# Kernel optimization log

Hardware: AMD Instinct MI355X
Metric: run time of the kernel (lower is better)

## Reference

```python
import jax, jax.numpy as jnp
import numpy as np
import math

NUM_HEADS = 8
LN_EPS = 1e-5


def layer_norm(x, g, b):
    mu = x.mean(-1, keepdims=True)
    var = ((x - mu) ** 2).mean(-1, keepdims=True)
    return (x - mu) * jax.lax.rsqrt(var + LN_EPS) * g + b


def typed_linear(x, W, types):
    # x: [E, in], W: [R, in, out], types: [E] int -> [E, out]
    out = jnp.zeros((x.shape[0], W.shape[-1]), x.dtype)
    for r in range(W.shape[0]):  # small fixed relation count
        out = out + jnp.where((types == r)[:, None], x @ W[r], 0.0)
    return out


def setup_inputs() -> dict:
    key = jax.random.key(0)
    ks = jax.random.split(key, 20)
    N, M, E = 50000, 10000, 100000
    in_dim, e_dim, out_dim, td = 128, 32, 128, 32
    R, T = 8, 4
    inp = {
        'src_h': jax.random.normal(ks[0], (N, in_dim), jnp.float32),
        'src_tw': jax.random.normal(ks[1], (N, td), jnp.float32),
        'src_tb': jax.random.normal(ks[2], (N, td), jnp.float32),
        'edge_h': jax.random.normal(ks[3], (E, e_dim), jnp.float32),
        'date': jax.random.uniform(ks[4], (E,), jnp.float32),
        'src_idx': jax.random.randint(ks[5], (E,), 0, N, jnp.int32),
        'dst_idx': jax.random.randint(ks[6], (E,), 0, M, jnp.int32),
        'etype': jax.random.randint(ks[7], (E,), 0, R, jnp.int32),
        'ntype': jax.random.randint(ks[8], (M,), 0, T, jnp.int32),
    }
    def w(k, shape):
        return jax.random.normal(k, shape, jnp.float32) / math.sqrt(shape[-2])
    inp['Wq'] = w(ks[9], (R, in_dim, out_dim))
    inp['Wk'] = w(ks[10], (R, in_dim + e_dim, out_dim))
    inp['Wv'] = w(ks[11], (R, in_dim + e_dim, out_dim))
    inp['Wa'] = w(ks[12], (T, out_dim, out_dim))
    inp['h_bias'] = jnp.zeros((T, out_dim), jnp.float32)
    inp['skip'] = jnp.ones((T,), jnp.float32)
    inp['src_ln_g'] = jnp.ones((in_dim + e_dim,), jnp.float32)
    inp['src_ln_b'] = jnp.zeros((in_dim + e_dim,), jnp.float32)
    inp['dst_ln_g'] = jnp.ones((in_dim,), jnp.float32)
    inp['dst_ln_b'] = jnp.zeros((in_dim,), jnp.float32)
    return inp


def reference(src_h, src_tw, src_tb, edge_h, date, src_idx, dst_idx, etype, ntype,
              Wq, Wk, Wv, Wa, h_bias, skip, src_ln_g, src_ln_b, dst_ln_g, dst_ln_b):
    M = ntype.shape[0]
    out_dim = Wq.shape[-1]
    H = NUM_HEADS
    hs = out_dim // H
    td = src_tw.shape[-1]
    t = date[:, None]  # [E,1]

    # gather src / dst node data per edge (dst nodes are first M src rows)
    h_s, tw_s, tb_s = src_h[src_idx], src_tw[src_idx], src_tb[src_idx]
    h_d, tw_d, tb_d = src_h[dst_idx], src_tw[dst_idx], src_tb[dst_idx]

    # time2vec modulation of the first td channels
    dia_s = jnp.concatenate([jnp.sin(tw_s * t + tb_s) * h_s[:, :td], h_s[:, td:]], -1)
    dia_d = jnp.concatenate([jnp.sin(tw_d * t + tb_d) * h_d[:, :td], h_d[:, td:]], -1)
    dia_s = jnp.concatenate([dia_s, edge_h], -1)  # [E, in_dim+e_dim]

    # pre_norm
    dia_s = layer_norm(dia_s, src_ln_g, src_ln_b)
    dia_d = layer_norm(dia_d, dst_ln_g, dst_ln_b)

    q = typed_linear(dia_d, Wq, etype).reshape(-1, H, hs)
    k = typed_linear(dia_s, Wk, etype).reshape(-1, H, hs)
    v = typed_linear(dia_s, Wv, etype).reshape(-1, H, hs)

    a = (q * k).sum(-1) / math.sqrt(out_dim)  # [E, H]

    # edge_softmax: segment softmax over destination nodes
    amax = jax.lax.stop_gradient(jax.ops.segment_max(a, dst_idx, num_segments=M))
    ex = jnp.exp(a - amax[dst_idx])
    denom = jax.ops.segment_sum(ex, dst_idx, num_segments=M)
    alpha = ex / denom[dst_idx]  # [E, H]

    # weighted scatter-sum aggregation
    m = (v * alpha[..., None]).reshape(-1, out_dim)  # [E, out_dim]
    h = jax.ops.segment_sum(m, dst_idx, num_segments=M)  # [M, out_dim]

    h = h + h_bias[ntype]
    gate = jax.nn.sigmoid(skip[ntype])[:, None]
    h = typed_linear(h, Wa, ntype)  # dropout is identity at eval
    dst_h = src_h[:M]
    return h * gate + dst_h * (1.0 - gate)
```

## Files before the change

### kernel.cpp

```cpp
#include <hip/hip_runtime.h>


typedef __attribute__((ext_vector_type(8))) short short8;
typedef __attribute__((ext_vector_type(4))) float f32x4;

__device__ __forceinline__ unsigned short f2bf(float f){
  union { float f; unsigned u; } x; x.f = f;
  unsigned r = x.u + 0x7FFFu + ((x.u >> 16) & 1u);
  return (unsigned short)(r >> 16);
}
__device__ __forceinline__ float bf2f(unsigned short b){
  union { unsigned u; float f; } x; x.u = ((unsigned)b) << 16;
  return x.f;
}
__device__ __forceinline__ float wred(float v){
  #pragma unroll
  for(int i=1;i<64;i<<=1) v += __shfl_xor(v, i);
  return v;
}


__global__ void k_zero(int* __restrict__ p, int n){
  int i = blockIdx.x*256 + threadIdx.x;
  if(i < n) p[i] = 0;
}

__global__ __launch_bounds__(256) void k_hist(
    const int* __restrict__ etype, const int* __restrict__ dst_idx,
    const int* __restrict__ ntype,
    int* cnt_e, int* cnt_d, int* cnt_n, int E, int M){
  __shared__ int le[8], ln[4];
  int tid = threadIdx.x;
  if(tid < 8) le[tid] = 0;
  if(tid < 4) ln[tid] = 0;
  __syncthreads();
  int g = blockIdx.x*256 + tid;
  if(g < E){ atomicAdd(&le[etype[g]], 1); atomicAdd(&cnt_d[dst_idx[g]], 1); }
  if(g < M){ atomicAdd(&ln[ntype[g]], 1); }
  __syncthreads();
  if(tid < 8 && le[tid]) atomicAdd(&cnt_e[tid], le[tid]);
  if(tid < 4 && ln[tid]) atomicAdd(&cnt_n[tid], ln[tid]);
}

__global__ __launch_bounds__(1024) void k_scan(const int* __restrict__ cnt_e, int* off_e,
                                               const int* __restrict__ cnt_n, int* off_n,
                                               const int* __restrict__ cnt_d, int* off_d, int M){
  __shared__ int part[1024];
  int tid = threadIdx.x;
  if(tid == 0){
    int s = 0;
    for(int i=0;i<8;i++){ off_e[i]=s; s+=cnt_e[i]; } off_e[8]=s;
    s = 0;
    for(int i=0;i<4;i++){ off_n[i]=s; s+=cnt_n[i]; } off_n[4]=s;
  }
  int per = (M + 1023) >> 10;
  int s = 0;
  for(int j=0;j<per;j++){ int idx = tid*per + j; if(idx < M) s += cnt_d[idx]; }
  part[tid] = s; __syncthreads();
  for(int o=1;o<1024;o<<=1){
    int v = (tid >= o) ? part[tid-o] : 0;
    __syncthreads();
    part[tid] += v;
    __syncthreads();
  }
  int run = (tid == 0) ? 0 : part[tid-1];
  for(int j=0;j<per;j++){
    int idx = tid*per + j;
    if(idx < M){ off_d[idx] = run; run += cnt_d[idx]; }
  }
  if(tid == 1023) off_d[M] = run;
}

__global__ __launch_bounds__(256) void k_scatter(
    const int* __restrict__ etype, const int* __restrict__ dst_idx,
    const int* __restrict__ ntype,
    const int* __restrict__ off_e, int* cur_e,
    const int* __restrict__ off_d, int* cur_d,
    const int* __restrict__ off_n, int* cur_n,
    int* eperm, int* dstlist, int* nperm, int* npos, int E, int M){
  __shared__ int lcnt[8], lbase[8], lnc[4], lnb[4];
  int tid = threadIdx.x;
  if(tid < 8) lcnt[tid] = 0;
  if(tid < 4) lnc[tid] = 0;
  __syncthreads();
  int g = blockIdx.x*256 + tid;
  int r = 0, lrank = 0, t = 0, nrank = 0;
  bool inE = (g < E), inM = (g < M);
  if(inE){ r = etype[g]; lrank = atomicAdd(&lcnt[r], 1); }
  if(inM){ t = ntype[g]; nrank = atomicAdd(&lnc[t], 1); }
  __syncthreads();
  if(tid < 8 && lcnt[tid]) lbase[tid] = atomicAdd(&cur_e[tid], lcnt[tid]);
  if(tid < 4 && lnc[tid])  lnb[tid]   = atomicAdd(&cur_n[tid], lnc[tid]);
  __syncthreads();
  if(inE){
    int p = off_e[r] + lbase[r] + lrank;
    eperm[p] = g;
    int d = dst_idx[g];
    int q = off_d[d] + atomicAdd(&cur_d[d], 1);
    dstlist[q] = p;
  }
  if(inM){
    int np = off_n[t] + lnb[t] + nrank;
    npos[g] = np;
    nperm[np] = g;
  }
}

__global__ void k_convw(const float* __restrict__ Wq, const float* __restrict__ Wk,
                        const float* __restrict__ Wv, const float* __restrict__ Wa,
                        unsigned short* Wq_t, unsigned short* Wk_t,
                        unsigned short* Wv_t, unsigned short* Wa_t){
  int tid = blockIdx.x*256 + threadIdx.x;
  if(tid < 131072){
    int r = tid >> 14, rem = tid & 16383, i = rem >> 7, o = rem & 127;
    Wq_t[(r<<14) + (o<<7) + i] = f2bf(Wq[tid]);
  } else if(tid < 294912){
    int u = tid - 131072;
    int r = u / 20480, rem = u - r*20480, i = rem >> 7, o = rem & 127;
    Wk_t[r*20480 + o*160 + i] = f2bf(Wk[u]);
  } else if(tid < 458752){
    int u = tid - 294912;
    int r = u / 20480, rem = u - r*20480, i = rem >> 7, o = rem & 127;
    Wv_t[r*20480 + o*160 + i] = f2bf(Wv[u]);
  } else if(tid < 524288){
    int u = tid - 458752;
    int r = u >> 14, rem = u & 16383, i = rem >> 7, o = rem & 127;
    Wa_t[(r<<14) + (o<<7) + i] = f2bf(Wa[u]);
  }
}

__global__ __launch_bounds__(256) void k_prep(
  const float* __restrict__ src_h, const float* __restrict__ src_tw, const float* __restrict__ src_tb,
  const float* __restrict__ edge_h, const float* __restrict__ date,
  const int* __restrict__ src_idx, const int* __restrict__ dst_idx, const int* __restrict__ eperm,
  const float* __restrict__ g_s, const float* __restrict__ b_s,
  const float* __restrict__ g_d, const float* __restrict__ b_d,
  unsigned short* __restrict__ dia_s, unsigned short* __restrict__ dia_d, int E)
{
  int p = blockIdx.x*4 + (threadIdx.x >> 6);
  if(p >= E) return;
  int lane = threadIdx.x & 63;
  int e = eperm[p];
  float t = date[e];
  int s = src_idx[e], d = dst_idx[e];
  {
    float h0 = src_h[(size_t)s*128 + lane];
    float h1 = src_h[(size_t)s*128 + 64 + lane];
    float x0 = h0, x2 = 0.f;
    if(lane < 32){
      x0 = __sinf(src_tw[s*32 + lane]*t + src_tb[s*32 + lane]) * h0;
      x2 = edge_h[(size_t)e*32 + lane];
    }
    float x1 = h1;
    float mu = wred(x0 + x1 + x2) * (1.f/160.f);
    float d0 = x0-mu, d1 = x1-mu, d2 = (lane<32) ? (x2-mu) : 0.f;
    float var = wred(d0*d0 + d1*d1 + d2*d2) * (1.f/160.f);
    float sc = rsqrtf(var + 1e-5f);
    size_t bo = (size_t)p*160;
    dia_s[bo + lane]      = f2bf(d0*sc*g_s[lane]      + b_s[lane]);
    dia_s[bo + 64 + lane] = f2bf(d1*sc*g_s[64+lane]   + b_s[64+lane]);
    if(lane < 32)
      dia_s[bo + 128 + lane] = f2bf(d2*sc*g_s[128+lane] + b_s[128+lane]);
  }
  {
    float h0 = src_h[(size_t)d*128 + lane];
    float h1 = src_h[(size_t)d*128 + 64 + lane];
    float x0 = (lane < 32) ? __sinf(src_tw[d*32+lane]*t + src_tb[d*32+lane]) * h0 : h0;
    float x1 = h1;
    float mu = wred(x0 + x1) * (1.f/128.f);
    float d0 = x0-mu, d1 = x1-mu;
    float var = wred(d0*d0 + d1*d1) * (1.f/128.f);
    float sc = rsqrtf(var + 1e-5f);
    size_t bo = (size_t)p*128;
    dia_d[bo + lane]      = f2bf(d0*sc*g_d[lane]    + b_d[lane]);
    dia_d[bo + 64 + lane] = f2bf(d1*sc*g_d[64+lane] + b_d[64+lane]);
  }
}

__device__ __forceinline__ void gemm64(
  const unsigned short* __restrict__ A, int lda,
  const unsigned short* __restrict__ Wg, int Kd,
  unsigned short* __restrict__ Bt, f32x4* acc, int tid)
{
  int lane = tid & 63, w = tid >> 6, m = lane & 15, quad = lane >> 4;
  #pragma unroll
  for(int i=0;i<8;i++) acc[i] = (f32x4){0.f,0.f,0.f,0.f};
  for(int k0=0; k0<Kd; k0+=32){
    __syncthreads();
    #pragma unroll
    for(int j=0;j<2;j++){
      int idx = j*256 + tid;
      int n = idx >> 2, qc = idx & 3;
      *(int4*)(Bt + n*40 + qc*8) = *(const int4*)(Wg + (size_t)n*Kd + k0 + qc*8);
    }
    __syncthreads();
    short8 b0 = *(const short8*)(Bt + (w*32 +      m)*40 + quad*8);
    short8 b1 = *(const short8*)(Bt + (w*32 + 16 + m)*40 + quad*8);
    #pragma unroll
    for(int rt=0; rt<4; rt++){
      short8 af = *(const short8*)(A + (rt*16 + m)*lda + k0 + quad*8);
      acc[rt*2+0] = __builtin_amdgcn_mfma_f32_16x16x32_bf16(af, b0, acc[rt*2+0], 0,0,0);
      acc[rt*2+1] = __builtin_amdgcn_mfma_f32_16x16x32_bf16(af, b1, acc[rt*2+1], 0,0,0);
    }
  }
}

__global__ __launch_bounds__(256) void k_qkv(
  const unsigned short* __restrict__ dia_d, const unsigned short* __restrict__ dia_s,
  const unsigned short* __restrict__ Wq_t, const unsigned short* __restrict__ Wk_t,
  const unsigned short* __restrict__ Wv_t,
  const int* __restrict__ cnt_e, const int* __restrict__ off_e,
  float* __restrict__ abuf, unsigned short* __restrict__ vbuf)
{
  __shared__ unsigned short Ad[64*136];
  __shared__ unsigned short As[64*168];
  __shared__ unsigned short Bt[128*40];
  int bid = blockIdx.x;
  int r = -1, tl0 = 0, accT = 0;
  #pragma unroll
  for(int i=0;i<8;i++){
    int n = cnt_e[i], tt = (n + 63) >> 6;
    if(r < 0 && bid < accT + tt){ r = i; tl0 = bid - accT; }
    accT += tt;
  }
  if(r < 0) return;
  int row0 = off_e[r] + tl0*64;
  int nv = min(64, cnt_e[r] - tl0*64);
  int tid = threadIdx.x;
  {
    int4 z = make_int4(0,0,0,0);
    #pragma unroll
    for(int it=0; it<4; it++){
      int idx = it*256 + tid, row = idx >> 4, c = idx & 15;
      int4 v = z;
      if(row < nv) v = *(const int4*)(dia_d + (size_t)(row0+row)*128 + c*8);
      *(int4*)(Ad + row*136 + c*8) = v;
    }
    #pragma unroll
    for(int it=0; it<5; it++){
      int idx = it*256 + tid, row = idx/20, c = idx%20;
      int4 v = z;
      if(row < nv) v = *(const int4*)(dia_s + (size_t)(row0+row)*160 + c*8);
      *(int4*)(As + row*168 + c*8) = v;
    }
  }
  int lane = tid & 63, w = tid >> 6, m = lane & 15, quad = lane >> 4;
  f32x4 q[8], kk[8], vv[8];
  gemm64(Ad, 136, Wq_t + r*16384, 128, Bt, q,  tid);
  gemm64(As, 168, Wk_t + r*20480, 160, Bt, kk, tid);
  const float inv = 0.08838834764831845f;
  #pragma unroll
  for(int rt=0; rt<4; rt++)
  #pragma unroll
  for(int ct=0; ct<2; ct++){
    #pragma unroll
    for(int reg=0; reg<4; reg++){
      float s = q[rt*2+ct][reg] * kk[rt*2+ct][reg];
      s += __shfl_xor(s,1); s += __shfl_xor(s,2); s += __shfl_xor(s,4); s += __shfl_xor(s,8);
      int row = rt*16 + quad*4 + reg;
      if(m == 0 && row < nv) abuf[(size_t)(row0+row)*8 + w*2 + ct] = s * inv;
    }
  }
  gemm64(As, 168, Wv_t + r*20480, 160, Bt, vv, tid);
  #pragma unroll
  for(int rt=0; rt<4; rt++)
  #pragma unroll
  for(int ct=0; ct<2; ct++)
  #pragma unroll
  for(int reg=0; reg<4; reg++){
    int row = rt*16 + quad*4 + reg;
    if(row < nv)
      vbuf[(size_t)(row0+row)*128 + w*32 + ct*16 + m] = f2bf(vv[rt*2+ct][reg]);
  }
}

__global__ __launch_bounds__(128) void k_aggr(
  const float* __restrict__ abuf, const unsigned short* __restrict__ vbuf,
  const int* __restrict__ dstlist, const int* __restrict__ off_d,
  const int* __restrict__ npos, const int* __restrict__ ntype,
  const float* __restrict__ h_bias, unsigned short* __restrict__ hpre)
{
  int d = blockIdx.x, tid = threadIdx.x;
  int o0 = off_d[d], cnt = off_d[d+1] - o0;
  __shared__ float den[8];
  if(tid < 8) den[tid] = 0.f;
  __syncthreads();
  for(int idx = tid; idx < cnt*8; idx += 128){
    int i = idx >> 3, h = idx & 7;
    float ex = __expf(abuf[(size_t)dstlist[o0+i]*8 + h]);
    atomicAdd(&den[h], ex);
  }
  __syncthreads();
  int h = tid >> 4;
  float dh = den[h];
  float rd = (dh > 0.f) ? (1.f/dh) : 0.f;
  float acc = 0.f;
  for(int i=0; i<cnt; i++){
    int p = dstlist[o0+i];
    float al = __expf(abuf[(size_t)p*8 + h]) * rd;
    acc += al * bf2f(vbuf[(size_t)p*128 + tid]);
  }
  int t = ntype[d];
  acc += h_bias[t*128 + tid];
  hpre[(size_t)npos[d]*128 + tid] = f2bf(acc);
}

__global__ __launch_bounds__(256) void k_final(
  const unsigned short* __restrict__ hpre, const unsigned short* __restrict__ Wa_t,
  const int* __restrict__ cnt_n, const int* __restrict__ off_n, const int* __restrict__ nperm,
  const float* __restrict__ skip, const float* __restrict__ src_h, float* __restrict__ out)
{
  __shared__ unsigned short Ah[64*136];
  __shared__ unsigned short Bt[128*40];
  int bid = blockIdx.x;
  int r = -1, tl0 = 0, accT = 0;
  #pragma unroll
  for(int i=0;i<4;i++){
    int n = cnt_n[i], tt = (n + 63) >> 6;
    if(r < 0 && bid < accT + tt){ r = i; tl0 = bid - accT; }
    accT += tt;
  }
  if(r < 0) return;
  int row0 = off_n[r] + tl0*64;
  int nv = min(64, cnt_n[r] - tl0*64);
  float gate = 1.f / (1.f + __expf(-skip[r]));
  int tid = threadIdx.x;
  int4 z = make_int4(0,0,0,0);
  #pragma unroll
  for(int it=0; it<4; it++){
    int idx = it*256 + tid, row = idx >> 4, c = idx & 15;
    int4 v = z;
    if(row < nv) v = *(const int4*)(hpre + (size_t)(row0+row)*128 + c*8);
    *(int4*)(Ah + row*136 + c*8) = v;
  }
  f32x4 acc[8];
  gemm64(Ah, 136, Wa_t + r*16384, 128, Bt, acc, tid);
  int lane = tid & 63, w = tid >> 6, m = lane & 15, quad = lane >> 4;
  #pragma unroll
  for(int rt=0; rt<4; rt++)
  #pragma unroll
  for(int ct=0; ct<2; ct++)
  #pragma unroll
  for(int reg=0; reg<4; reg++){
    int row = rt*16 + quad*4 + reg;
    if(row < nv){
      int dd = nperm[row0+row];
      int col = w*32 + ct*16 + m;
      out[(size_t)dd*128 + col] = acc[rt*2+ct][reg]*gate + src_h[(size_t)dd*128 + col]*(1.f - gate);
    }
  }
}

extern "C" void kernel_launch(void* const* d_in, const int* in_sizes, int n_in,
                              void* d_out, int out_size, void* d_ws, size_t ws_size,
                              hipStream_t stream)
{
  const float* src_h  = (const float*)d_in[0];
  const float* src_tw = (const float*)d_in[1];
  const float* src_tb = (const float*)d_in[2];
  const float* edge_h = (const float*)d_in[3];
  const float* date   = (const float*)d_in[4];
  const int*   src_idx= (const int*)d_in[5];
  const int*   dst_idx= (const int*)d_in[6];
  const int*   etype  = (const int*)d_in[7];
  const int*   ntype  = (const int*)d_in[8];
  const float* Wq     = (const float*)d_in[9];
  const float* Wk     = (const float*)d_in[10];
  const float* Wv     = (const float*)d_in[11];
  const float* Wa     = (const float*)d_in[12];
  const float* h_bias = (const float*)d_in[13];
  const float* skip   = (const float*)d_in[14];
  const float* g_s    = (const float*)d_in[15];
  const float* b_s    = (const float*)d_in[16];
  const float* g_d    = (const float*)d_in[17];
  const float* b_d    = (const float*)d_in[18];
  float* out = (float*)d_out;

  const int E = in_sizes[4];
  const int M = in_sizes[8];

  char* base = (char*)d_ws;
  size_t off = 0;
  auto alloc = [&](size_t bytes)->char*{
    off = (off + 255) & ~(size_t)255;
    char* p = base + off; off += bytes; return p;
  };
  int* cnt_e = (int*)alloc((size_t)(24 + 2*M)*4);
  int* cur_e = cnt_e + 8;
  int* cnt_n = cur_e + 8;
  int* cur_n = cnt_n + 4;
  int* cnt_d = cur_n + 4;
  int* cur_d = cnt_d + M;
  const int nzero = 24 + 2*M;
  int* off_e = (int*)alloc(9*4);
  int* off_n = (int*)alloc(5*4);
  int* off_d = (int*)alloc((size_t)(M+1)*4);
  int* eperm   = (int*)alloc((size_t)E*4);
  int* dstlist = (int*)alloc((size_t)E*4);
  int* nperm   = (int*)alloc((size_t)M*4);
  int* npos    = (int*)alloc((size_t)M*4);
  unsigned short* Wq_t = (unsigned short*)alloc((size_t)8*128*128*2);
  unsigned short* Wk_t = (unsigned short*)alloc((size_t)8*160*128*2);
  unsigned short* Wv_t = (unsigned short*)alloc((size_t)8*160*128*2);
  unsigned short* Wa_t = (unsigned short*)alloc((size_t)4*128*128*2);
  unsigned short* dia_d = (unsigned short*)alloc((size_t)E*128*2);
  unsigned short* dia_s = (unsigned short*)alloc((size_t)E*160*2);
  unsigned short* vbuf  = (unsigned short*)alloc((size_t)E*128*2);
  unsigned short* hpre  = (unsigned short*)alloc((size_t)M*128*2);
  float* abuf = (float*)alloc((size_t)E*8*4);

  k_zero<<<dim3((nzero+255)/256), dim3(256), 0, stream>>>(cnt_e, nzero);
  k_hist<<<dim3((E+255)/256), dim3(256), 0, stream>>>(etype, dst_idx, ntype, cnt_e, cnt_d, cnt_n, E, M);
  k_scan<<<dim3(1), dim3(1024), 0, stream>>>(cnt_e, off_e, cnt_n, off_n, cnt_d, off_d, M);
  k_scatter<<<dim3((E+255)/256), dim3(256), 0, stream>>>(etype, dst_idx, ntype,
      off_e, cur_e, off_d, cur_d, off_n, cur_n, eperm, dstlist, nperm, npos, E, M);
  k_convw<<<dim3(2048), dim3(256), 0, stream>>>(Wq, Wk, Wv, Wa, Wq_t, Wk_t, Wv_t, Wa_t);
  k_prep<<<dim3((E+3)/4), dim3(256), 0, stream>>>(src_h, src_tw, src_tb, edge_h, date,
      src_idx, dst_idx, eperm, g_s, b_s, g_d, b_d, dia_s, dia_d, E);
  k_qkv<<<dim3(E/64 + 9), dim3(256), 0, stream>>>(dia_d, dia_s, Wq_t, Wk_t, Wv_t,
      cnt_e, off_e, abuf, vbuf);
  k_aggr<<<dim3(M), dim3(128), 0, stream>>>(abuf, vbuf, dstlist, off_d, npos, ntype, h_bias, hpre);
  k_final<<<dim3(M/64 + 5), dim3(256), 0, stream>>>(hpre, Wa_t, cnt_n, off_n, nperm, skip, src_h, out);
}
```

Measured before the change: 289.8 us.

## Pre-swizzle weights into MFMA fragment layout and load B directly to registers

The weight conversion kernel now writes bf16 weights in the exact per-lane MFMA B-fragment order. The GEMM helper can then load all B fragments straight from global memory into registers with coalesced 16-byte loads, with no LDS staging. This drops the shared-memory B tile and the two barriers per K-step. It adds register pressure, since up to 10 short8 fragments are held per GEMM, and relies on weights being L2-resident across blocks.

```diff
diff --git a/kernel.cpp b/kernel.cpp
--- a/kernel.cpp
+++ b/kernel.cpp
@@ -112,20 +112,24 @@
                         unsigned short* Wv_t, unsigned short* Wa_t){
   int tid = blockIdx.x*256 + threadIdx.x;
   if(tid < 131072){
-    int r = tid >> 14, rem = tid & 16383, i = rem >> 7, o = rem & 127;
-    Wq_t[(r<<14) + (o<<7) + i] = f2bf(Wq[tid]);
+    int r = tid >> 14, rem = tid & 16383, k = rem >> 7, n = rem & 127;
+    int nb=n>>4, m=n&15, c=k>>5, quad=(k>>3)&3, j=k&7;
+    Wq_t[r*16384 + ((nb*4 + c)*4 + quad)*128 + m*8 + j] = f2bf(Wq[tid]);
   } else if(tid < 294912){
     int u = tid - 131072;
-    int r = u / 20480, rem = u - r*20480, i = rem >> 7, o = rem & 127;
-    Wk_t[r*20480 + o*160 + i] = f2bf(Wk[u]);
+    int r = u / 20480, rem = u - r*20480, k = rem >> 7, n = rem & 127;
+    int nb=n>>4, m=n&15, c=k>>5, quad=(k>>3)&3, j=k&7;
+    Wk_t[r*20480 + ((nb*5 + c)*4 + quad)*128 + m*8 + j] = f2bf(Wk[u]);
   } else if(tid < 458752){
     int u = tid - 294912;
-    int r = u / 20480, rem = u - r*20480, i = rem >> 7, o = rem & 127;
-    Wv_t[r*20480 + o*160 + i] = f2bf(Wv[u]);
+    int r = u / 20480, rem = u - r*20480, k = rem >> 7, n = rem & 127;
+    int nb=n>>4, m=n&15, c=k>>5, quad=(k>>3)&3, j=k&7;
+    Wv_t[r*20480 + ((nb*5 + c)*4 + quad)*128 + m*8 + j] = f2bf(Wv[u]);
   } else if(tid < 524288){
     int u = tid - 458752;
-    int r = u >> 14, rem = u & 16383, i = rem >> 7, o = rem & 127;
-    Wa_t[(r<<14) + (o<<7) + i] = f2bf(Wa[u]);
+    int r = u >> 14, rem = u & 16383, k = rem >> 7, n = rem & 127;
+    int nb=n>>4, m=n&15, c=k>>5, quad=(k>>3)&3, j=k&7;
+    Wa_t[r*16384 + ((nb*4 + c)*4 + quad)*128 + m*8 + j] = f2bf(Wa[u]);
   }
 }
 
@@ -177,30 +181,29 @@
   }
 }
 
-__device__ __forceinline__ void gemm64(
+template<int NC>
+__device__ __forceinline__ void gemm64r(
   const unsigned short* __restrict__ A, int lda,
-  const unsigned short* __restrict__ Wg, int Kd,
-  unsigned short* __restrict__ Bt, f32x4* acc, int tid)
+  const unsigned short* __restrict__ Wf,
+  f32x4* acc, int tid)
 {
   int lane = tid & 63, w = tid >> 6, m = lane & 15, quad = lane >> 4;
+  const unsigned short* p0 = Wf + (size_t)(2*w)*NC*512 + lane*8;
+  short8 b0[NC], b1[NC];
+  #pragma unroll
+  for(int c=0;c<NC;c++){
+    b0[c] = *(const short8*)(p0 + c*512);
+    b1[c] = *(const short8*)(p0 + NC*512 + c*512);
+  }
   #pragma unroll
   for(int i=0;i<8;i++) acc[i] = (f32x4){0.f,0.f,0.f,0.f};
-  for(int k0=0; k0<Kd; k0+=32){
-    __syncthreads();
-    #pragma unroll
-    for(int j=0;j<2;j++){
-      int idx = j*256 + tid;
-      int n = idx >> 2, qc = idx & 3;
-      *(int4*)(Bt + n*40 + qc*8) = *(const int4*)(Wg + (size_t)n*Kd + k0 + qc*8);
-    }
-    __syncthreads();
-    short8 b0 = *(const short8*)(Bt + (w*32 +      m)*40 + quad*8);
-    short8 b1 = *(const short8*)(Bt + (w*32 + 16 + m)*40 + quad*8);
+  #pragma unroll
+  for(int c=0;c<NC;c++){
     #pragma unroll
     for(int rt=0; rt<4; rt++){
-      short8 af = *(const short8*)(A + (rt*16 + m)*lda + k0 + quad*8);
-      acc[rt*2+0] = __builtin_amdgcn_mfma_f32_16x16x32_bf16(af, b0, acc[rt*2+0], 0,0,0);
-      acc[rt*2+1] = __builtin_amdgcn_mfma_f32_16x16x32_bf16(af, b1, acc[rt*2+1], 0,0,0);
+      short8 af = *(const short8*)(A + (rt*16 + m)*lda + c*32 + quad*8);
+      acc[rt*2+0] = __builtin_amdgcn_mfma_f32_16x16x32_bf16(af, b0[c], acc[rt*2+0], 0,0,0);
+      acc[rt*2+1] = __builtin_amdgcn_mfma_f32_16x16x32_bf16(af, b1[c], acc[rt*2+1], 0,0,0);
     }
   }
 }
@@ -214,7 +217,6 @@
 {
   __shared__ unsigned short Ad[64*136];
   __shared__ unsigned short As[64*168];
-  __shared__ unsigned short Bt[128*40];
   int bid = blockIdx.x;
   int r = -1, tl0 = 0, accT = 0;
   #pragma unroll
@@ -244,10 +246,11 @@
       *(int4*)(As + row*168 + c*8) = v;
     }
   }
+  __syncthreads();
   int lane = tid & 63, w = tid >> 6, m = lane & 15, quad = lane >> 4;
   f32x4 q[8], kk[8], vv[8];
-  gemm64(Ad, 136, Wq_t + r*16384, 128, Bt, q,  tid);
-  gemm64(As, 168, Wk_t + r*20480, 160, Bt, kk, tid);
+  gemm64r<4>(Ad, 136, Wq_t + r*16384, q,  tid);
+  gemm64r<5>(As, 168, Wk_t + r*20480, kk, tid);
   const float inv = 0.08838834764831845f;
   #pragma unroll
   for(int rt=0; rt<4; rt++)
@@ -261,7 +264,7 @@
       if(m == 0 && row < nv) abuf[(size_t)(row0+row)*8 + w*2 + ct] = s * inv;
     }
   }
-  gemm64(As, 168, Wv_t + r*20480, 160, Bt, vv, tid);
+  gemm64r<5>(As, 168, Wv_t + r*20480, vv, tid);
   #pragma unroll
   for(int rt=0; rt<4; rt++)
   #pragma unroll
@@ -311,7 +314,6 @@
   const float* __restrict__ skip, const float* __restrict__ src_h, float* __restrict__ out)
 {
   __shared__ unsigned short Ah[64*136];
-  __shared__ unsigned short Bt[128*40];
   int bid = blockIdx.x;
   int r = -1, tl0 = 0, accT = 0;
   #pragma unroll
@@ -333,8 +335,9 @@
     if(row < nv) v = *(const int4*)(hpre + (size_t)(row0+row)*128 + c*8);
     *(int4*)(Ah + row*136 + c*8) = v;
   }
+  __syncthreads();
   f32x4 acc[8];
-  gemm64(Ah, 136, Wa_t + r*16384, 128, Bt, acc, tid);
+  gemm64r<4>(Ah, 136, Wa_t + r*16384, acc, tid);
   int lane = tid & 63, w = tid >> 6, m = lane & 15, quad = lane >> 4;
   #pragma unroll
   for(int rt=0; rt<4; rt++)
```

New measurement: 284.8 us. About the same (-1.7%).
